# Kernel optimization log

Hardware: AMD Instinct MI355X
Metric: run time of the kernel (lower is better)

Reference implementation:

```python
import jax, jax.numpy as jnp
import numpy as np

EPS = 1e-6
NEG = 1e9

def _norm(x):
    # Normalizator math with alpha=1, gamma=0 (torch.std is unbiased -> ddof=1)
    m = jnp.mean(x, axis=-1, keepdims=True)
    s = jnp.std(x, axis=-1, ddof=1, keepdims=True)
    return (x - m) / (s + EPS)

def setup_inputs() -> dict:
    key = jax.random.key(0)
    ks = jax.random.split(key, 16)
    T, S, D, F, L = 4096, 4096, 512, 2048, 4
    sc = 1.0 / np.sqrt(D)
    scf = 1.0 / np.sqrt(F)
    return {
        "current_tgt_output": jax.random.normal(ks[0], (T, D), jnp.float32),
        "encoder_output": jax.random.normal(ks[1], (S, D), jnp.float32),
        "cross_mask": jax.random.randint(ks[2], (T, S), 0, 2).astype(jnp.float32),
        "Wq": jax.random.normal(ks[3], (L, D, D), jnp.float32) * sc,
        "Wk": jax.random.normal(ks[4], (L, D, D), jnp.float32) * sc,
        "Wv": jax.random.normal(ks[5], (L, D, D), jnp.float32) * sc,
        "Wo": jax.random.normal(ks[6], (L, D, D), jnp.float32) * sc,
        "Cq": jax.random.normal(ks[7], (L, D, D), jnp.float32) * sc,
        "Ck": jax.random.normal(ks[8], (L, D, D), jnp.float32) * sc,
        "Cv": jax.random.normal(ks[9], (L, D, D), jnp.float32) * sc,
        "Co": jax.random.normal(ks[10], (L, D, D), jnp.float32) * sc,
        "W1": jax.random.normal(ks[11], (L, D, F), jnp.float32) * sc,
        "W2": jax.random.normal(ks[12], (L, F, D), jnp.float32) * scf,
        "alpha": jnp.ones((1,), jnp.float32),
        "gamma": jnp.zeros((1,), jnp.float32),
        "input_ids": jax.random.randint(ks[13], (T,), 0, S),
        "training_step": T,
        "training_mode": 1,
    }

def reference(current_tgt_output, encoder_output, cross_mask, Wq, Wk, Wv, Wo,
              Cq, Ck, Cv, Co, W1, W2, alpha, gamma, input_ids,
              training_step, training_mode):
    T = training_step
    x = current_tgt_output[:T] if training_mode else current_tgt_output
    cm = cross_mask[:T]                                  # [T, S]
    # the python double-loop -> single vectorized gather: self_mask[i,k]=cross_mask[i, input_ids[k]]
    self_mask = cm[:, input_ids]                         # [T, T]
    sbias = (self_mask - 1.0) * NEG                      # additive mask bias
    cbias = (cm - 1.0) * NEG
    D = x.shape[-1]
    scale = 1.0 / jnp.sqrt(jnp.asarray(D, x.dtype))
    L = Wq.shape[0]
    for l in range(L):
        h = _norm(x)
        q, k, v = h @ Wq[l], h @ Wk[l], h @ Wv[l]
        a = jax.nn.softmax(q @ k.T * scale + sbias, axis=-1)
        x = x + (a @ v) @ Wo[l]
        h = _norm(x)
        q = h @ Cq[l]
        k, v = encoder_output @ Ck[l], encoder_output @ Cv[l]
        a = jax.nn.softmax(q @ k.T * scale + cbias, axis=-1)
        x = x + (a @ v) @ Co[l]
        h = _norm(x)
        x = x + jax.nn.relu(h @ W1[l]) @ W2[l]
    return alpha * _norm(x) + gamma
```

## Files before the change

kernel.cpp:

```cpp
#include <hip/hip_runtime.h>
#include <math.h>

typedef _Float16 half_t;
typedef unsigned int u32;
typedef unsigned short u16;
typedef float f32x4 __attribute__((ext_vector_type(4)));
typedef _Float16 f16x8 __attribute__((ext_vector_type(8)));
typedef _Float16 f16x4 __attribute__((ext_vector_type(4)));

#define T_DIM 4096
#define S_DIM 4096
#define D_DIM 512
#define F_DIM 2048
#define NLAYER 4

__device__ __forceinline__ void gload16(const void* g, void* l) {
    __builtin_amdgcn_global_load_lds(
        (const __attribute__((address_space(1))) u32*)g,
        (__attribute__((address_space(3))) u32*)l, 16, 0, 0);
}

template<int N> __device__ __forceinline__ void wait_vm() {
    if constexpr (N == 0) asm volatile("s_waitcnt vmcnt(0)" ::: "memory");
    else if constexpr (N == 3) asm volatile("s_waitcnt vmcnt(3)" ::: "memory");
    else if constexpr (N == 4) asm volatile("s_waitcnt vmcnt(4)" ::: "memory");
    else if constexpr (N == 6) asm volatile("s_waitcnt vmcnt(6)" ::: "memory");
    else if constexpr (N == 8) asm volatile("s_waitcnt vmcnt(8)" ::: "memory");
}

template<int BN, int EPI, int SPLITK = 1>
__global__ __launch_bounds__(512)
void gemm_nt(const half_t* __restrict__ A, int lda,
             const half_t* __restrict__ B, int ldb,
             int N, int K, int gx,
             const float* __restrict__ Cin, float* __restrict__ Cout,
             half_t* __restrict__ D1, half_t* __restrict__ D2,
             half_t* __restrict__ D3, int ldd)
{
    constexpr int BM = 128, BK = 64;
    constexpr int NF = BN / 32;
    constexpr int LPT = 2 + BN / 64;
    constexpr int NSLOT = (BN == 64) ? 3 : 2;
    __shared__ half_t As[NSLOT][BM * BK];
    __shared__ half_t Bs[NSLOT][BN * BK];

    const int tid  = threadIdx.x;
    const int wave = tid >> 6;
    const int lane = tid & 63;

    const int nb  = gridDim.x;
    const int bid = blockIdx.x;
    const int nid = (bid & 7) * (nb >> 3) + (bid >> 3);
    const int gy  = nb / (gx * SPLITK);
    const int bx  = nid % gx;
    const int tmp = nid / gx;
    const int by  = tmp % gy;
    const int kz  = tmp / gy;
    const int bm = by * BM, bn = bx * BN;

    const int Keff = K / SPLITK;
    A += (size_t)kz * Keff;
    B += (size_t)kz * Keff;

    const int wm = (wave >> 1) * 32;
    const int wn = (wave & 1) * (BN / 2);
    const int kq = lane >> 4;
    const int rr = lane & 15;
    const int scol = (((lane & 7) ^ (lane >> 3)) << 3);

    f32x4 acc[2][NF];
#pragma unroll
    for (int m = 0; m < 2; ++m)
#pragma unroll
        for (int n = 0; n < NF; ++n)
            acc[m][n] = f32x4{0.f, 0.f, 0.f, 0.f};

    auto stage = [&](int buf, int k0) {
#pragma unroll
        for (int c = 0; c < 2; ++c) {
            const int row = wave * 16 + c * 8 + (lane >> 3);
            gload16(A + (size_t)(bm + row) * lda + k0 + scol,
                    (char*)&As[buf][0] + (wave * 2 + c) * 1024 + lane * 16);
        }
        if constexpr (BN == 64) {
            const int row = wave * 8 + (lane >> 3);
            gload16(B + (size_t)(bn + row) * ldb + k0 + scol,
                    (char*)&Bs[buf][0] + wave * 1024 + lane * 16);
        } else {
#pragma unroll
            for (int c = 0; c < 2; ++c) {
                const int row = wave * 16 + c * 8 + (lane >> 3);
                gload16(B + (size_t)(bn + row) * ldb + k0 + scol,
                        (char*)&Bs[buf][0] + (wave * 2 + c) * 1024 + lane * 16);
            }
        }
    };

    const int nt = Keff / BK;
    stage(0, 0);
    if constexpr (NSLOT == 3) stage(1, BK);
    int cur = 0, pf = NSLOT - 1;
    for (int t = 0; t < nt; ++t) {
        if (t + 1 < nt) wait_vm<(NSLOT - 2) * LPT>(); else wait_vm<0>();
        __builtin_amdgcn_s_barrier();
        if (t + NSLOT - 1 < nt) stage(pf, (t + NSLOT - 1) * BK);
#pragma unroll
        for (int ks = 0; ks < 2; ++ks) {
            f16x8 af[2], bf[NF];
#pragma unroll
            for (int m = 0; m < 2; ++m) {
                const int r = wm + m * 16 + rr;
                af[m] = *(const f16x8*)&As[cur][r * BK + (((ks * 4 + kq) ^ (r & 7)) << 3)];
            }
#pragma unroll
            for (int n = 0; n < NF; ++n) {
                const int r = wn + n * 16 + rr;
                bf[n] = *(const f16x8*)&Bs[cur][r * BK + (((ks * 4 + kq) ^ (r & 7)) << 3)];
            }
#pragma unroll
            for (int m = 0; m < 2; ++m)
#pragma unroll
                for (int n = 0; n < NF; ++n)
                    acc[m][n] = __builtin_amdgcn_mfma_f32_16x16x32_f16(af[m], bf[n], acc[m][n], 0, 0, 0);
        }
        cur = (cur + 1 == NSLOT) ? 0 : cur + 1;
        pf  = (pf  + 1 == NSLOT) ? 0 : pf  + 1;
    }

    const int r0 = bm + wm + (lane >> 4) * 4;
#pragma unroll
    for (int m = 0; m < 2; ++m)
#pragma unroll
        for (int n = 0; n < NF; ++n) {
            const int c = bn + wn + n * 16 + rr;
            if constexpr (SPLITK > 1) {
                float* Cp = Cout + (size_t)kz * gy * BM * N;
#pragma unroll
                for (int i = 0; i < 4; ++i)
                    Cp[(size_t)(r0 + m * 16 + i) * N + c] = acc[m][n][i];
            } else if (EPI == 0 || EPI == 1) {
#pragma unroll
                for (int i = 0; i < 4; ++i) {
                    const int r = r0 + m * 16 + i;
                    const float v = acc[m][n][i];
                    Cout[(size_t)r * N + c] = (EPI == 1) ? (Cin[(size_t)r * N + c] + v) : v;
                }
            } else if (EPI == 2 || EPI == 4) {
#pragma unroll
                for (int i = 0; i < 4; ++i) {
                    float v = acc[m][n][i];
                    if (EPI == 4) v = fmaxf(v, 0.f);
                    D1[(size_t)(r0 + m * 16 + i) * ldd + c] = (half_t)v;
                }
            } else if (EPI == 5) {
                if (bn < 512) {
#pragma unroll
                    for (int i = 0; i < 4; ++i)
                        D1[(size_t)(r0 + m * 16 + i) * 512 + c] = (half_t)acc[m][n][i];
                } else if (bn < 1024) {
#pragma unroll
                    for (int i = 0; i < 4; ++i)
                        D2[(size_t)(r0 + m * 16 + i) * 512 + (c - 512)] = (half_t)acc[m][n][i];
                } else {
                    f16x4 hv;
#pragma unroll
                    for (int i = 0; i < 4; ++i) hv[i] = (half_t)acc[m][n][i];
                    *(f16x4*)&D3[(size_t)(c - 1024) * ldd + r0 + m * 16] = hv;
                }
            } else {
                if (bn < 512) {
#pragma unroll
                    for (int i = 0; i < 4; ++i)
                        D2[(size_t)(r0 + m * 16 + i) * 512 + c] = (half_t)acc[m][n][i];
                } else {
                    f16x4 hv;
#pragma unroll
                    for (int i = 0; i < 4; ++i) hv[i] = (half_t)acc[m][n][i];
                    *(f16x4*)&D3[(size_t)(c - 512) * ldd + r0 + m * 16] = hv;
                }
            }
        }
}

template<int EPI>
__global__ __launch_bounds__(256)
void gemm97(const half_t* __restrict__ A, int lda,
            const half_t* __restrict__ B, int ldb,
            int K, int gx, half_t* __restrict__ D, int ldd)
{
    constexpr int BK = 32, NSLOT = 3, LPT = 4;
    __shared__ half_t As[NSLOT][128 * BK];
    __shared__ half_t Bs[NSLOT][128 * BK];

    const int tid  = threadIdx.x;
    const int wave = tid >> 6;
    const int lane = tid & 63;

    const int nb  = gridDim.x;
    const int bid = blockIdx.x;
    const int nid = (bid & 7) * (nb >> 3) + (bid >> 3);
    const int bx = nid % gx, by = nid / gx;
    const int bm = by * 128, bn = bx * 128;

    const int wm = (wave >> 1) * 64;
    const int wn = (wave & 1) * 64;
    const int kq = lane >> 4;
    const int rr = lane & 15;
    const int srow = lane >> 2;
    const int scol = (((lane & 3) ^ ((lane >> 3) & 3)) << 3);
    const int kqa  = kq ^ ((rr >> 1) & 3);

    const half_t* Abase = A + (size_t)(bm + wave * 16 + srow) * lda + scol;
    const half_t* Bbase = B + (size_t)(bn + wave * 16 + srow) * ldb + scol;

    f32x4 acc[4][4];
#pragma unroll
    for (int m = 0; m < 4; ++m)
#pragma unroll
        for (int n = 0; n < 4; ++n)
            acc[m][n] = f32x4{0.f, 0.f, 0.f, 0.f};

    auto stage = [&](int buf, int k0) {
#pragma unroll
        for (int c = 0; c < 2; ++c)
            gload16(Abase + (size_t)c * 64 * lda + k0,
                    (char*)&As[buf][0] + c * 4096 + wave * 1024 + lane * 16);
#pragma unroll
        for (int c = 0; c < 2; ++c)
            gload16(Bbase + (size_t)c * 64 * ldb + k0,
                    (char*)&Bs[buf][0] + c * 4096 + wave * 1024 + lane * 16);
    };

    const int nt = K / BK;
    stage(0, 0);
    stage(1, BK);
    int cur = 0, pf = 2;
    for (int t = 0; t < nt; ++t) {
        if (t + 1 < nt) wait_vm<LPT>(); else wait_vm<0>();
        __builtin_amdgcn_s_barrier();
        if (t + 2 < nt) stage(pf, (t + 2) * BK);
        f16x8 af[4], bf[4];
#pragma unroll
        for (int m = 0; m < 4; ++m)
            af[m] = *(const f16x8*)&As[cur][(wm + m * 16 + rr) * BK + kqa * 8];
#pragma unroll
        for (int n = 0; n < 4; ++n)
            bf[n] = *(const f16x8*)&Bs[cur][(wn + n * 16 + rr) * BK + kqa * 8];
#pragma unroll
        for (int m = 0; m < 4; ++m)
#pragma unroll
            for (int n = 0; n < 4; ++n)
                acc[m][n] = __builtin_amdgcn_mfma_f32_16x16x32_f16(af[m], bf[n], acc[m][n], 0, 0, 0);
        cur = (cur == 2) ? 0 : cur + 1;
        pf  = (pf  == 2) ? 0 : pf + 1;
    }

    const int r0 = bm + wm + (lane >> 4) * 4;
#pragma unroll
    for (int m = 0; m < 4; ++m)
#pragma unroll
        for (int n = 0; n < 4; ++n) {
            const int c = bn + wn + n * 16 + rr;
#pragma unroll
            for (int i = 0; i < 4; ++i) {
                float v = acc[m][n][i];
                if (EPI == 4) v = fmaxf(v, 0.f);
                D[(size_t)(r0 + m * 16 + i) * ldd + c] = (half_t)v;
            }
        }
}

template<int NS, int MODE>
__global__ __launch_bounds__(256)
void reduce_splitk(const float* __restrict__ P, const float* __restrict__ Cin,
                   float* __restrict__ Cout, half_t* __restrict__ D)
{
    const size_t MN = (size_t)T_DIM * 512;
    const size_t i = ((size_t)blockIdx.x * 256 + threadIdx.x) * 8;
    float s[8];
    {
        float4 a = *(const float4*)&P[i];
        float4 b = *(const float4*)&P[i + 4];
        s[0] = a.x; s[1] = a.y; s[2] = a.z; s[3] = a.w;
        s[4] = b.x; s[5] = b.y; s[6] = b.z; s[7] = b.w;
    }
#pragma unroll
    for (int k = 1; k < NS; ++k) {
        float4 a = *(const float4*)&P[k * MN + i];
        float4 b = *(const float4*)&P[k * MN + i + 4];
        s[0] += a.x; s[1] += a.y; s[2] += a.z; s[3] += a.w;
        s[4] += b.x; s[5] += b.y; s[6] += b.z; s[7] += b.w;
    }
    if (MODE == 0) {
        f16x8 o;
#pragma unroll
        for (int j = 0; j < 8; ++j) o[j] = (half_t)s[j];
        *(f16x8*)&D[i] = o;
    } else {
        float4 c0 = *(const float4*)&Cin[i];
        float4 c1 = *(const float4*)&Cin[i + 4];
        float4 o0 = {c0.x + s[0], c0.y + s[1], c0.z + s[2], c0.w + s[3]};
        float4 o1 = {c1.x + s[4], c1.y + s[5], c1.z + s[6], c1.w + s[7]};
        *(float4*)&Cout[i] = o0;
        *(float4*)&Cout[i + 4] = o1;
    }
}

template<int FINAL>
__global__ __launch_bounds__(256)
void norm_rows(const float* __restrict__ x, half_t* __restrict__ hh,
               float* __restrict__ outF, const float* __restrict__ alphaP,
               const float* __restrict__ gammaP)
{
    const int row  = blockIdx.x * 4 + (threadIdx.x >> 6);
    const int lane = threadIdx.x & 63;
    const float* xr = x + (size_t)row * D_DIM + lane * 8;
    float4 a = *(const float4*)xr;
    float4 b = *(const float4*)(xr + 4);
    float v[8] = {a.x, a.y, a.z, a.w, b.x, b.y, b.z, b.w};
    float s = 0.f;
#pragma unroll
    for (int j = 0; j < 8; ++j) s += v[j];
#pragma unroll
    for (int off = 32; off; off >>= 1) s += __shfl_xor(s, off);
    const float mean = s * (1.f / 512.f);
    float ss = 0.f;
#pragma unroll
    for (int j = 0; j < 8; ++j) { float d = v[j] - mean; ss += d * d; }
#pragma unroll
    for (int off = 32; off; off >>= 1) ss += __shfl_xor(ss, off);
    const float inv = 1.f / (sqrtf(ss * (1.f / 511.f)) + 1e-6f);
    if (FINAL) {
        const float alp = alphaP[0], gam = gammaP[0];
        float o[8];
#pragma unroll
        for (int j = 0; j < 8; ++j) o[j] = alp * ((v[j] - mean) * inv) + gam;
        float4 o0 = {o[0], o[1], o[2], o[3]};
        float4 o1 = {o[4], o[5], o[6], o[7]};
        float* op = outF + (size_t)row * D_DIM + lane * 8;
        *(float4*)op = o0;
        *(float4*)(op + 4) = o1;
    } else {
        f16x8 hv;
#pragma unroll
        for (int j = 0; j < 8; ++j) hv[j] = (half_t)((v[j] - mean) * inv);
        *(f16x8*)&hh[(size_t)row * D_DIM + lane * 8] = hv;
    }
}

__global__ __launch_bounds__(256)
void cast_f16(const float* __restrict__ in, half_t* __restrict__ out)
{
    size_t i = ((size_t)blockIdx.x * 256 + threadIdx.x) * 8;
    float4 a = *(const float4*)&in[i];
    float4 b = *(const float4*)&in[i + 4];
    float v[8] = {a.x, a.y, a.z, a.w, b.x, b.y, b.z, b.w};
    f16x8 o;
#pragma unroll
    for (int j = 0; j < 8; ++j) o[j] = (half_t)v[j];
    *(f16x8*)&out[i] = o;
}

__global__ __launch_bounds__(256)
void transpose_cast(const float* __restrict__ in, half_t* __restrict__ out,
                    int R, int C, float scale, int inZ, int outZ)
{
    in  += (size_t)blockIdx.z * inZ;
    out += (size_t)blockIdx.z * outZ;
    __shared__ float tile[32][33];
    const int tx = threadIdx.x & 31, ty = threadIdx.x >> 5;
    const int r0 = blockIdx.y * 32, c0 = blockIdx.x * 32;
#pragma unroll
    for (int i = 0; i < 4; ++i)
        tile[ty + i * 8][tx] = in[(size_t)(r0 + ty + i * 8) * C + c0 + tx];
    __syncthreads();
#pragma unroll
    for (int i = 0; i < 4; ++i)
        out[(size_t)(c0 + ty + i * 8) * R + r0 + tx] = (half_t)(tile[tx][ty + i * 8] * scale);
}

__global__ __launch_bounds__(256)
void pack_masks(const float* __restrict__ cm, const int* __restrict__ ids,
                u32* __restrict__ crossb, u32* __restrict__ selfb)
{
    const int t = blockIdx.x;
    const float* row = cm + (size_t)t * S_DIM;
    __shared__ u32 cb[S_DIM / 32];
    __shared__ u16 sh16[256];
    const int tid = threadIdx.x;
    u32 bits = 0;
#pragma unroll
    for (int q = 0; q < 4; ++q) {
        float4 v = *(const float4*)&row[tid * 16 + q * 4];
        bits |= (v.x > 0.5f ? 1u : 0u) << (q * 4 + 0);
        bits |= (v.y > 0.5f ? 1u : 0u) << (q * 4 + 1);
        bits |= (v.z > 0.5f ? 1u : 0u) << (q * 4 + 2);
        bits |= (v.w > 0.5f ? 1u : 0u) << (q * 4 + 3);
    }
    ((u16*)cb)[tid] = (u16)bits;
    __syncthreads();
    u32 sb = 0;
#pragma unroll
    for (int q = 0; q < 4; ++q) {
        int4 id4 = *(const int4*)&ids[tid * 16 + q * 4];
        sb |= ((cb[id4.x >> 5] >> (id4.x & 31)) & 1u) << (q * 4 + 0);
        sb |= ((cb[id4.y >> 5] >> (id4.y & 31)) & 1u) << (q * 4 + 1);
        sb |= ((cb[id4.z >> 5] >> (id4.z & 31)) & 1u) << (q * 4 + 2);
        sb |= ((cb[id4.w >> 5] >> (id4.w & 31)) & 1u) << (q * 4 + 3);
    }
    sh16[tid] = (u16)sb;
    __syncthreads();
    if (tid < 128) {
        crossb[(size_t)t * 128 + tid] = cb[tid];
        selfb[(size_t)t * 128 + tid]  = (u32)sh16[2 * tid] | ((u32)sh16[2 * tid + 1] << 16);
    }
}

__global__ __launch_bounds__(256)
void softmax_rows16(half_t* __restrict__ logits, const u32* __restrict__ bits)
{
    const int t = blockIdx.x;
    half_t* row = logits + (size_t)t * S_DIM;
    const u32* bw = bits + (size_t)t * (S_DIM / 32);
    __shared__ float red[8];
    const int tid = threadIdx.x, wave = tid >> 6, lane = tid & 63;
    const int s0 = tid * 16;
    f16x8 h0 = *(const f16x8*)&row[s0];
    f16x8 h1 = *(const f16x8*)&row[s0 + 8];
    const u32 w = bw[tid >> 1] >> ((tid & 1) * 16);
    float z[16];
    float lmax = -3.0e38f;
#pragma unroll
    for (int q = 0; q < 16; ++q) {
        const float v = (float)((q < 8) ? h0[q & 7] : h1[q & 7]);
        z[q] = v + (((w >> q) & 1u) ? 0.f : -1e9f);
        lmax = fmaxf(lmax, z[q]);
    }
#pragma unroll
    for (int off = 32; off; off >>= 1) lmax = fmaxf(lmax, __shfl_xor(lmax, off));
    if (lane == 0) red[wave] = lmax;
    __syncthreads();
    const float mx = fmaxf(fmaxf(red[0], red[1]), fmaxf(red[2], red[3]));
    float lsum = 0.f;
#pragma unroll
    for (int q = 0; q < 16; ++q) { z[q] = __expf(z[q] - mx); lsum += z[q]; }
#pragma unroll
    for (int off = 32; off; off >>= 1) lsum += __shfl_xor(lsum, off);
    if (lane == 0) red[4 + wave] = lsum;
    __syncthreads();
    const float inv = 1.f / (red[4] + red[5] + red[6] + red[7]);
    f16x8 o0, o1;
#pragma unroll
    for (int q = 0; q < 8; ++q) {
        o0[q] = (half_t)(z[q] * inv);
        o1[q] = (half_t)(z[q + 8] * inv);
    }
    *(f16x8*)&row[s0] = o0;
    *(f16x8*)&row[s0 + 8] = o1;
}

extern "C" void kernel_launch(void* const* d_in, const int* in_sizes, int n_in,
                              void* d_out, int out_size, void* d_ws, size_t ws_size,
                              hipStream_t stream)
{
    (void)in_sizes; (void)n_in; (void)out_size; (void)ws_size;

    const float* x0p  = (const float*)d_in[0];
    const float* encp = (const float*)d_in[1];
    const float* cmp  = (const float*)d_in[2];
    const float* Wq = (const float*)d_in[3], *Wk = (const float*)d_in[4];
    const float* Wv = (const float*)d_in[5], *Wo = (const float*)d_in[6];
    const float* Cq = (const float*)d_in[7], *Ck = (const float*)d_in[8];
    const float* Cv = (const float*)d_in[9], *Co = (const float*)d_in[10];
    const float* W1p = (const float*)d_in[11];
    const float* W2p = (const float*)d_in[12];
    const float* alphap = (const float*)d_in[13];
    const float* gammap = (const float*)d_in[14];
    const int*   idsp   = (const int*)d_in[15];
    float* outp = (float*)d_out;

    char* wp = (char*)d_ws;
    auto take = [&](size_t nelem, int esz) -> void* {
        void* p = (void*)wp;
        wp += (nelem * (size_t)esz + 255) & ~(size_t)255;
        return p;
    };
    half_t* wqkvT = (half_t*)take((size_t)NLAYER * 1536 * 512, 2);
    half_t* ckvT  = (half_t*)take((size_t)NLAYER * 1024 * 512, 2);
    half_t* cqT   = (half_t*)take((size_t)NLAYER * 512 * 512, 2);
    half_t* woT   = (half_t*)take((size_t)NLAYER * 512 * 512, 2);
    half_t* coT   = (half_t*)take((size_t)NLAYER * 512 * 512, 2);
    half_t* w1T   = (half_t*)take((size_t)NLAYER * D_DIM * F_DIM, 2);
    half_t* w2T   = (half_t*)take((size_t)NLAYER * D_DIM * F_DIM, 2);
    half_t* hh    = (half_t*)take((size_t)T_DIM * D_DIM, 2);
    half_t* qb    = (half_t*)take((size_t)T_DIM * D_DIM, 2);
    half_t* kb    = (half_t*)take((size_t)S_DIM * D_DIM, 2);
    half_t* vT    = (half_t*)take((size_t)S_DIM * D_DIM, 2);
    half_t* ao    = (half_t*)take((size_t)T_DIM * D_DIM, 2);
    half_t* mid   = (half_t*)take((size_t)T_DIM * F_DIM, 2);
    half_t* enc16 = (half_t*)take((size_t)S_DIM * D_DIM, 2);
    float* xbuf   = (float*)take((size_t)T_DIM * D_DIM, 4);
    half_t* logit16 = (half_t*)take((size_t)T_DIM * S_DIM, 2);
    float* pbuf   = (float*)take((size_t)4 * T_DIM * D_DIM, 4);
    u32* crossb = (u32*)take((size_t)T_DIM * (S_DIM / 32), 4);
    u32* selfb  = (u32*)take((size_t)T_DIM * (S_DIM / 32), 4);

    const dim3 B(256), B512(512);
    const float qscale = 0.04419417382415922f;

    const int SQ = 512 * 512, QKVZ = 1536 * 512, KVZ = 1024 * 512, FZ = 512 * 2048;
    transpose_cast<<<dim3(16,16,4), B, 0, stream>>>(Wq, wqkvT,            512, 512, qscale, SQ, QKVZ);
    transpose_cast<<<dim3(16,16,4), B, 0, stream>>>(Wk, wqkvT + SQ,       512, 512, 1.f,    SQ, QKVZ);
    transpose_cast<<<dim3(16,16,4), B, 0, stream>>>(Wv, wqkvT + 2 * SQ,   512, 512, 1.f,    SQ, QKVZ);
    transpose_cast<<<dim3(16,16,4), B, 0, stream>>>(Wo, woT,              512, 512, 1.f,    SQ, SQ);
    transpose_cast<<<dim3(16,16,4), B, 0, stream>>>(Cq, cqT,              512, 512, qscale, SQ, SQ);
    transpose_cast<<<dim3(16,16,4), B, 0, stream>>>(Ck, ckvT,             512, 512, 1.f,    SQ, KVZ);
    transpose_cast<<<dim3(16,16,4), B, 0, stream>>>(Cv, ckvT + SQ,        512, 512, 1.f,    SQ, KVZ);
    transpose_cast<<<dim3(16,16,4), B, 0, stream>>>(Co, coT,              512, 512, 1.f,    SQ, SQ);
    transpose_cast<<<dim3(64,16,4), B, 0, stream>>>(W1p, w1T, 512, 2048, 1.f, FZ, FZ);
    transpose_cast<<<dim3(16,64,4), B, 0, stream>>>(W2p, w2T, 2048, 512, 1.f, FZ, FZ);
    cast_f16<<<dim3((S_DIM * D_DIM / 8) / 256), B, 0, stream>>>(encp, enc16);
    pack_masks<<<dim3(T_DIM), B, 0, stream>>>(cmp, idsp, crossb, selfb);

    const dim3 gRED(T_DIM * D_DIM / 8 / 256);

    for (int l = 0; l < NLAYER; ++l) {
        const float* xin = (l == 0) ? x0p : xbuf;

        norm_rows<0><<<T_DIM / 4, B, 0, stream>>>(xin, hh, nullptr, nullptr, nullptr);
        gemm_nt<64, 5><<<dim3(768), B512, 0, stream>>>(hh, 512, wqkvT + (size_t)l * QKVZ, 512,
            1536, 512, 24, nullptr, nullptr, qb, kb, vT, 4096);
        gemm97<2><<<dim3(1024), B, 0, stream>>>(qb, 512, kb, 512,
            512, 32, logit16, 4096);
        softmax_rows16<<<dim3(T_DIM), B, 0, stream>>>(logit16, selfb);
        gemm_nt<64, 0, 4><<<dim3(1024), B512, 0, stream>>>(logit16, 4096, vT, 4096,
            512, 4096, 8, nullptr, pbuf, nullptr, nullptr, nullptr, 0);
        reduce_splitk<4, 0><<<gRED, B, 0, stream>>>(pbuf, nullptr, nullptr, ao);
        gemm_nt<64, 1><<<dim3(256), B512, 0, stream>>>(ao, 512, woT + (size_t)l * SQ, 512,
            512, 512, 8, xin, xbuf, nullptr, nullptr, nullptr, 0);

        norm_rows<0><<<T_DIM / 4, B, 0, stream>>>(xbuf, hh, nullptr, nullptr, nullptr);
        gemm_nt<64, 2><<<dim3(256), B512, 0, stream>>>(hh, 512, cqT + (size_t)l * SQ, 512,
            512, 512, 8, nullptr, nullptr, qb, nullptr, nullptr, 512);
        gemm_nt<64, 6><<<dim3(512), B512, 0, stream>>>(enc16, 512, ckvT + (size_t)l * KVZ, 512,
            1024, 512, 16, nullptr, nullptr, nullptr, kb, vT, 4096);
        gemm97<2><<<dim3(1024), B, 0, stream>>>(qb, 512, kb, 512,
            512, 32, logit16, 4096);
        softmax_rows16<<<dim3(T_DIM), B, 0, stream>>>(logit16, crossb);
        gemm_nt<64, 0, 4><<<dim3(1024), B512, 0, stream>>>(logit16, 4096, vT, 4096,
            512, 4096, 8, nullptr, pbuf, nullptr, nullptr, nullptr, 0);
        reduce_splitk<4, 0><<<gRED, B, 0, stream>>>(pbuf, nullptr, nullptr, ao);
        gemm_nt<64, 1><<<dim3(256), B512, 0, stream>>>(ao, 512, coT + (size_t)l * SQ, 512,
            512, 512, 8, xbuf, xbuf, nullptr, nullptr, nullptr, 0);

        norm_rows<0><<<T_DIM / 4, B, 0, stream>>>(xbuf, hh, nullptr, nullptr, nullptr);
        gemm97<4><<<dim3(512), B, 0, stream>>>(hh, 512, w1T + (size_t)l * FZ, 512,
            512, 16, mid, 2048);
        gemm_nt<64, 0, 2><<<dim3(512), B512, 0, stream>>>(mid, 2048, w2T + (size_t)l * FZ, 2048,
            512, 2048, 8, nullptr, pbuf, nullptr, nullptr, nullptr, 0);
        reduce_splitk<2, 1><<<gRED, B, 0, stream>>>(pbuf, xbuf, xbuf, nullptr);
    }

    norm_rows<1><<<T_DIM / 4, B, 0, stream>>>(xbuf, nullptr, outp, alphap, gammap);
}
```

Baseline: 1.107 ms.

## Hoist cross-attention KV projections, use 128x128 split-K GEMMs with fused reduce-norm

```diff
diff --git a/kernel.cpp b/kernel.cpp
--- a/kernel.cpp
+++ b/kernel.cpp
@@ -13,6 +13,7 @@
 #define D_DIM 512
 #define F_DIM 2048
 #define NLAYER 4
+#define KVS ((size_t)4096 * 512)
 
 __device__ __forceinline__ void gload16(const void* g, void* l) {
     __builtin_amdgcn_global_load_lds(
@@ -28,7 +29,7 @@
     else if constexpr (N == 8) asm volatile("s_waitcnt vmcnt(8)" ::: "memory");
 }
 
-template<int BN, int EPI, int SPLITK = 1>
+template<int BN, int EPI>
 __global__ __launch_bounds__(512)
 void gemm_nt(const half_t* __restrict__ A, int lda,
              const half_t* __restrict__ B, int ldb,
@@ -51,16 +52,10 @@
     const int nb  = gridDim.x;
     const int bid = blockIdx.x;
     const int nid = (bid & 7) * (nb >> 3) + (bid >> 3);
-    const int gy  = nb / (gx * SPLITK);
+    const int gy  = nb / gx;
     const int bx  = nid % gx;
-    const int tmp = nid / gx;
-    const int by  = tmp % gy;
-    const int kz  = tmp / gy;
+    const int by  = nid / gx % gy;
     const int bm = by * BM, bn = bx * BN;
-
-    const int Keff = K / SPLITK;
-    A += (size_t)kz * Keff;
-    B += (size_t)kz * Keff;
 
     const int wm = (wave >> 1) * 32;
     const int wn = (wave & 1) * (BN / 2);
@@ -96,7 +91,7 @@
         }
     };
 
-    const int nt = Keff / BK;
+    const int nt = K / BK;
     stage(0, 0);
     if constexpr (NSLOT == 3) stage(1, BK);
     int cur = 0, pf = NSLOT - 1;
@@ -133,25 +128,16 @@
 #pragma unroll
         for (int n = 0; n < NF; ++n) {
             const int c = bn + wn + n * 16 + rr;
-            if constexpr (SPLITK > 1) {
-                float* Cp = Cout + (size_t)kz * gy * BM * N;
-#pragma unroll
-                for (int i = 0; i < 4; ++i)
-                    Cp[(size_t)(r0 + m * 16 + i) * N + c] = acc[m][n][i];
-            } else if (EPI == 0 || EPI == 1) {
+            if (EPI == 1) {
 #pragma unroll
                 for (int i = 0; i < 4; ++i) {
                     const int r = r0 + m * 16 + i;
-                    const float v = acc[m][n][i];
-                    Cout[(size_t)r * N + c] = (EPI == 1) ? (Cin[(size_t)r * N + c] + v) : v;
+                    Cout[(size_t)r * N + c] = Cin[(size_t)r * N + c] + acc[m][n][i];
                 }
-            } else if (EPI == 2 || EPI == 4) {
-#pragma unroll
-                for (int i = 0; i < 4; ++i) {
-                    float v = acc[m][n][i];
-                    if (EPI == 4) v = fmaxf(v, 0.f);
-                    D1[(size_t)(r0 + m * 16 + i) * ldd + c] = (half_t)v;
-                }
+            } else if (EPI == 2) {
+#pragma unroll
+                for (int i = 0; i < 4; ++i)
+                    D1[(size_t)(r0 + m * 16 + i) * ldd + c] = (half_t)acc[m][n][i];
             } else if (EPI == 5) {
                 if (bn < 512) {
 #pragma unroll
@@ -168,25 +154,28 @@
                     *(f16x4*)&D3[(size_t)(c - 1024) * ldd + r0 + m * 16] = hv;
                 }
             } else {
-                if (bn < 512) {
+                const int l = c >> 10;
+                const int sub = c & 1023;
+                if (sub < 512) {
 #pragma unroll
                     for (int i = 0; i < 4; ++i)
-                        D2[(size_t)(r0 + m * 16 + i) * 512 + c] = (half_t)acc[m][n][i];
+                        D2[l * KVS + (size_t)(r0 + m * 16 + i) * 512 + sub] = (half_t)acc[m][n][i];
                 } else {
                     f16x4 hv;
 #pragma unroll
                     for (int i = 0; i < 4; ++i) hv[i] = (half_t)acc[m][n][i];
-                    *(f16x4*)&D3[(size_t)(c - 512) * ldd + r0 + m * 16] = hv;
+                    *(f16x4*)&D3[l * KVS + (size_t)(sub - 512) * 4096 + r0 + m * 16] = hv;
                 }
             }
         }
 }
 
-template<int EPI>
+template<int EPI, int SPLITK = 1, int P16 = 1>
 __global__ __launch_bounds__(256)
 void gemm97(const half_t* __restrict__ A, int lda,
             const half_t* __restrict__ B, int ldb,
-            int K, int gx, half_t* __restrict__ D, int ldd)
+            int K, int gx, half_t* __restrict__ D,
+            float* __restrict__ Fout, int ldd)
 {
     constexpr int BK = 32, NSLOT = 3, LPT = 4;
     __shared__ half_t As[NSLOT][128 * BK];
@@ -199,8 +188,16 @@
     const int nb  = gridDim.x;
     const int bid = blockIdx.x;
     const int nid = (bid & 7) * (nb >> 3) + (bid >> 3);
-    const int bx = nid % gx, by = nid / gx;
+    const int gy  = nb / (gx * SPLITK);
+    const int bx  = nid % gx;
+    const int tmp = nid / gx;
+    const int by  = tmp % gy;
+    const int kz  = tmp / gy;
     const int bm = by * 128, bn = bx * 128;
+
+    const int Keff = K / SPLITK;
+    A += (size_t)kz * Keff;
+    B += (size_t)kz * Keff;
 
     const int wm = (wave >> 1) * 64;
     const int wn = (wave & 1) * 64;
@@ -231,7 +228,7 @@
                     (char*)&Bs[buf][0] + c * 4096 + wave * 1024 + lane * 16);
     };
 
-    const int nt = K / BK;
+    const int nt = Keff / BK;
     stage(0, 0);
     stage(1, BK);
     int cur = 0, pf = 2;
@@ -256,6 +253,7 @@
     }
 
     const int r0 = bm + wm + (lane >> 4) * 4;
+    const int soff = kz * gx * 128;
 #pragma unroll
     for (int m = 0; m < 4; ++m)
 #pragma unroll
@@ -264,45 +262,91 @@
 #pragma unroll
             for (int i = 0; i < 4; ++i) {
                 float v = acc[m][n][i];
-                if (EPI == 4) v = fmaxf(v, 0.f);
-                D[(size_t)(r0 + m * 16 + i) * ldd + c] = (half_t)v;
+                const size_t r = r0 + m * 16 + i;
+                if constexpr (SPLITK > 1) {
+                    if constexpr (P16) D[r * ldd + soff + c] = (half_t)v;
+                    else               Fout[r * ldd + soff + c] = v;
+                } else {
+                    if (EPI == 4) v = fmaxf(v, 0.f);
+                    D[r * ldd + c] = (half_t)v;
+                }
             }
         }
 }
 
-template<int NS, int MODE>
-__global__ __launch_bounds__(256)
-void reduce_splitk(const float* __restrict__ P, const float* __restrict__ Cin,
-                   float* __restrict__ Cout, half_t* __restrict__ D)
-{
-    const size_t MN = (size_t)T_DIM * 512;
-    const size_t i = ((size_t)blockIdx.x * 256 + threadIdx.x) * 8;
-    float s[8];
+__global__ __launch_bounds__(256)
+void reduce_p16(const half_t* __restrict__ P, half_t* __restrict__ ao)
+{
+    const size_t q = ((size_t)blockIdx.x * 256 + threadIdx.x) * 8;
+    const size_t r = q >> 9;
+    const int d = (int)(q & 511);
+    const half_t* row = P + r * 2048 + d;
+    float s[8] = {0.f};
+#pragma unroll
+    for (int j = 0; j < 4; ++j) {
+        f16x8 v = *(const f16x8*)(row + j * 512);
+#pragma unroll
+        for (int e = 0; e < 8; ++e) s[e] += (float)v[e];
+    }
+    f16x8 o;
+#pragma unroll
+    for (int e = 0; e < 8; ++e) o[e] = (half_t)s[e];
+    *(f16x8*)&ao[q] = o;
+}
+
+template<int FINAL>
+__global__ __launch_bounds__(256)
+void norm_red(const float* __restrict__ xin, const float* __restrict__ P,
+              float* __restrict__ xbuf, half_t* __restrict__ hh,
+              float* __restrict__ outF, const float* __restrict__ alphaP,
+              const float* __restrict__ gammaP)
+{
+    const int row  = blockIdx.x * 4 + (threadIdx.x >> 6);
+    const int lane = threadIdx.x & 63;
+    const int d0 = lane * 8;
+    const float* xr = xin + (size_t)row * D_DIM + d0;
+    float v[8];
     {
-        float4 a = *(const float4*)&P[i];
-        float4 b = *(const float4*)&P[i + 4];
-        s[0] = a.x; s[1] = a.y; s[2] = a.z; s[3] = a.w;
-        s[4] = b.x; s[5] = b.y; s[6] = b.z; s[7] = b.w;
-    }
-#pragma unroll
-    for (int k = 1; k < NS; ++k) {
-        float4 a = *(const float4*)&P[k * MN + i];
-        float4 b = *(const float4*)&P[k * MN + i + 4];
-        s[0] += a.x; s[1] += a.y; s[2] += a.z; s[3] += a.w;
-        s[4] += b.x; s[5] += b.y; s[6] += b.z; s[7] += b.w;
-    }
-    if (MODE == 0) {
-        f16x8 o;
-#pragma unroll
-        for (int j = 0; j < 8; ++j) o[j] = (half_t)s[j];
-        *(f16x8*)&D[i] = o;
+        float4 a = *(const float4*)xr;
+        float4 b = *(const float4*)(xr + 4);
+        v[0]=a.x; v[1]=a.y; v[2]=a.z; v[3]=a.w; v[4]=b.x; v[5]=b.y; v[6]=b.z; v[7]=b.w;
+    }
+    const float* pr = P + (size_t)row * 2048 + d0;
+#pragma unroll
+    for (int j = 0; j < 4; ++j) {
+        float4 a = *(const float4*)(pr + j * 512);
+        float4 b = *(const float4*)(pr + j * 512 + 4);
+        v[0]+=a.x; v[1]+=a.y; v[2]+=a.z; v[3]+=a.w; v[4]+=b.x; v[5]+=b.y; v[6]+=b.z; v[7]+=b.w;
+    }
+    float* xo = xbuf + (size_t)row * D_DIM + d0;
+    *(float4*)xo       = float4{v[0], v[1], v[2], v[3]};
+    *(float4*)(xo + 4) = float4{v[4], v[5], v[6], v[7]};
+
+    float s = 0.f;
+#pragma unroll
+    for (int j = 0; j < 8; ++j) s += v[j];
+#pragma unroll
+    for (int off = 32; off; off >>= 1) s += __shfl_xor(s, off);
+    const float mean = s * (1.f / 512.f);
+    float ss = 0.f;
+#pragma unroll
+    for (int j = 0; j < 8; ++j) { float d = v[j] - mean; ss += d * d; }
+#pragma unroll
+    for (int off = 32; off; off >>= 1) ss += __shfl_xor(ss, off);
+    const float inv = 1.f / (sqrtf(ss * (1.f / 511.f)) + 1e-6f);
+    if (FINAL) {
+        const float alp = alphaP[0], gam = gammaP[0];
+        float o[8];
+#pragma unroll
+        for (int j = 0; j < 8; ++j) o[j] = alp * ((v[j] - mean) * inv) + gam;
+        float* op = outF + (size_t)row * D_DIM + d0;
+        *(float4*)op       = float4{o[0], o[1], o[2], o[3]};
+        *(float4*)(op + 4) = float4{o[4], o[5], o[6], o[7]};
     } else {
-        float4 c0 = *(const float4*)&Cin[i];
-        float4 c1 = *(const float4*)&Cin[i + 4];
-        float4 o0 = {c0.x + s[0], c0.y + s[1], c0.z + s[2], c0.w + s[3]};
-        float4 o1 = {c1.x + s[4], c1.y + s[5], c1.z + s[6], c1.w + s[7]};
-        *(float4*)&Cout[i] = o0;
-        *(float4*)&Cout[i + 4] = o1;
+        f16x8 hv;
+#pragma unroll
+        for (int j = 0; j < 8; ++j) hv[j] = (half_t)((v[j] - mean) * inv);
+        *(f16x8*)&hh[(size_t)row * D_DIM + d0] = hv;
     }
 }
 
@@ -335,11 +379,9 @@
         float o[8];
 #pragma unroll
         for (int j = 0; j < 8; ++j) o[j] = alp * ((v[j] - mean) * inv) + gam;
-        float4 o0 = {o[0], o[1], o[2], o[3]};
-        float4 o1 = {o[4], o[5], o[6], o[7]};
         float* op = outF + (size_t)row * D_DIM + lane * 8;
-        *(float4*)op = o0;
-        *(float4*)(op + 4) = o1;
+        *(float4*)op       = float4{o[0], o[1], o[2], o[3]};
+        *(float4*)(op + 4) = float4{o[4], o[5], o[6], o[7]};
     } else {
         f16x8 hv;
 #pragma unroll
@@ -499,9 +541,12 @@
     half_t* ao    = (half_t*)take((size_t)T_DIM * D_DIM, 2);
     half_t* mid   = (half_t*)take((size_t)T_DIM * F_DIM, 2);
     half_t* enc16 = (half_t*)take((size_t)S_DIM * D_DIM, 2);
+    half_t* kbC   = (half_t*)take((size_t)NLAYER * S_DIM * D_DIM, 2);
+    half_t* vTC   = (half_t*)take((size_t)NLAYER * S_DIM * D_DIM, 2);
     float* xbuf   = (float*)take((size_t)T_DIM * D_DIM, 4);
     half_t* logit16 = (half_t*)take((size_t)T_DIM * S_DIM, 2);
-    float* pbuf   = (float*)take((size_t)4 * T_DIM * D_DIM, 4);
+    half_t* p16   = (half_t*)take((size_t)T_DIM * 2048, 2);
+    float* pbuf   = (float*)take((size_t)T_DIM * 2048, 4);
     u32* crossb = (u32*)take((size_t)T_DIM * (S_DIM / 32), 4);
     u32* selfb  = (u32*)take((size_t)T_DIM * (S_DIM / 32), 4);
 
@@ -521,45 +566,45 @@
     transpose_cast<<<dim3(16,64,4), B, 0, stream>>>(W2p, w2T, 2048, 512, 1.f, FZ, FZ);
     cast_f16<<<dim3((S_DIM * D_DIM / 8) / 256), B, 0, stream>>>(encp, enc16);
     pack_masks<<<dim3(T_DIM), B, 0, stream>>>(cmp, idsp, crossb, selfb);
-
-    const dim3 gRED(T_DIM * D_DIM / 8 / 256);
+    gemm_nt<64, 7><<<dim3(2048), B512, 0, stream>>>(enc16, 512, ckvT, 512,
+        4096, 512, 64, nullptr, nullptr, nullptr, kbC, vTC, 4096);
 
     for (int l = 0; l < NLAYER; ++l) {
         const float* xin = (l == 0) ? x0p : xbuf;
 
-        norm_rows<0><<<T_DIM / 4, B, 0, stream>>>(xin, hh, nullptr, nullptr, nullptr);
+        if (l == 0)
+            norm_rows<0><<<T_DIM / 4, B, 0, stream>>>(x0p, hh, nullptr, nullptr, nullptr);
+        else
+            norm_red<0><<<T_DIM / 4, B, 0, stream>>>(xbuf, pbuf, xbuf, hh, nullptr, nullptr, nullptr);
+
         gemm_nt<64, 5><<<dim3(768), B512, 0, stream>>>(hh, 512, wqkvT + (size_t)l * QKVZ, 512,
             1536, 512, 24, nullptr, nullptr, qb, kb, vT, 4096);
-        gemm97<2><<<dim3(1024), B, 0, stream>>>(qb, 512, kb, 512,
-            512, 32, logit16, 4096);
+        gemm97<2><<<dim3(1024), B, 0, stream>>>(qb, 512, kb, 512, 512, 32, logit16, nullptr, 4096);
         softmax_rows16<<<dim3(T_DIM), B, 0, stream>>>(logit16, selfb);
-        gemm_nt<64, 0, 4><<<dim3(1024), B512, 0, stream>>>(logit16, 4096, vT, 4096,
-            512, 4096, 8, nullptr, pbuf, nullptr, nullptr, nullptr, 0);
-        reduce_splitk<4, 0><<<gRED, B, 0, stream>>>(pbuf, nullptr, nullptr, ao);
+        gemm97<0, 4, 1><<<dim3(512), B, 0, stream>>>(logit16, 4096, vT, 4096,
+            4096, 4, p16, nullptr, 2048);
+        reduce_p16<<<dim3(1024), B, 0, stream>>>(p16, ao);
         gemm_nt<64, 1><<<dim3(256), B512, 0, stream>>>(ao, 512, woT + (size_t)l * SQ, 512,
             512, 512, 8, xin, xbuf, nullptr, nullptr, nullptr, 0);
 
         norm_rows<0><<<T_DIM / 4, B, 0, stream>>>(xbuf, hh, nullptr, nullptr, nullptr);
         gemm_nt<64, 2><<<dim3(256), B512, 0, stream>>>(hh, 512, cqT + (size_t)l * SQ, 512,
             512, 512, 8, nullptr, nullptr, qb, nullptr, nullptr, 512);
-        gemm_nt<64, 6><<<dim3(512), B512, 0, stream>>>(enc16, 512, ckvT + (size_t)l * KVZ, 512,
-            1024, 512, 16, nullptr, nullptr, nullptr, kb, vT, 4096);
-        gemm97<2><<<dim3(1024), B, 0, stream>>>(qb, 512, kb, 512,
-            512, 32, logit16, 4096);
+        gemm97<2><<<dim3(1024), B, 0, stream>>>(qb, 512, kbC + (size_t)l * KVS, 512,
+            512, 32, logit16, nullptr, 4096);
         softmax_rows16<<<dim3(T_DIM), B, 0, stream>>>(logit16, crossb);
-        gemm_nt<64, 0, 4><<<dim3(1024), B512, 0, stream>>>(logit16, 4096, vT, 4096,
-            512, 4096, 8, nullptr, pbuf, nullptr, nullptr, nullptr, 0);
-        reduce_splitk<4, 0><<<gRED, B, 0, stream>>>(pbuf, nullptr, nullptr, ao);
+        gemm97<0, 4, 1><<<dim3(512), B, 0, stream>>>(logit16, 4096, vTC + (size_t)l * KVS, 4096,
+            4096, 4, p16, nullptr, 2048);
+        reduce_p16<<<dim3(1024), B, 0, stream>>>(p16, ao);
         gemm_nt<64, 1><<<dim3(256), B512, 0, stream>>>(ao, 512, coT + (size_t)l * SQ, 512,
             512, 512, 8, xbuf, xbuf, nullptr, nullptr, nullptr, 0);
 
         norm_rows<0><<<T_DIM / 4, B, 0, stream>>>(xbuf, hh, nullptr, nullptr, nullptr);
         gemm97<4><<<dim3(512), B, 0, stream>>>(hh, 512, w1T + (size_t)l * FZ, 512,
-            512, 16, mid, 2048);
-        gemm_nt<64, 0, 2><<<dim3(512), B512, 0, stream>>>(mid, 2048, w2T + (size_t)l * FZ, 2048,
-            512, 2048, 8, nullptr, pbuf, nullptr, nullptr, nullptr, 0);
-        reduce_splitk<2, 1><<<gRED, B, 0, stream>>>(pbuf, xbuf, xbuf, nullptr);
-    }
-
-    norm_rows<1><<<T_DIM / 4, B, 0, stream>>>(xbuf, nullptr, outp, alphap, gammap);
-}
+            512, 16, mid, nullptr, 2048);
+        gemm97<0, 4, 0><<<dim3(512), B, 0, stream>>>(mid, 2048, w2T + (size_t)l * FZ, 2048,
+            2048, 4, nullptr, pbuf, 2048);
+    }
+
+    norm_red<1><<<T_DIM / 4, B, 0, stream>>>(xbuf, pbuf, xbuf, nullptr, outp, alphap, gammap);
+}
```

After: 1.091 ms. Within noise of the previous version (-1.5%).
